# Kernel tuning notes

Measured on AMD Instinct MI355X. Metric: run time of the kernel, lower is better.

## Reference

```python
import jax, jax.numpy as jnp
import numpy as np

BS, C, H, W = 4, 128, 64, 64  # input_dim=128
INNER = 64


def setup_inputs() -> dict:
    key = jax.random.key(0)
    ks = jax.random.split(key, 9)
    s_in = 1.0 / np.sqrt(C)
    s_inner = 1.0 / np.sqrt(INNER)
    return {
        "inpt": jax.random.normal(ks[0], (BS, C, H, W), dtype=jnp.float32),
        "Wq": jax.random.normal(ks[1], (INNER, C), dtype=jnp.float32) * s_in,
        "bq": jax.random.normal(ks[2], (INNER,), dtype=jnp.float32) * 0.01,
        "Wk": jax.random.normal(ks[3], (INNER, C), dtype=jnp.float32) * s_in,
        "bk": jax.random.normal(ks[4], (INNER,), dtype=jnp.float32) * 0.01,
        "Wv": jax.random.normal(ks[5], (INNER, C), dtype=jnp.float32) * s_in,
        "bv": jax.random.normal(ks[6], (INNER,), dtype=jnp.float32) * 0.01,
        "Wo": jax.random.normal(ks[7], (C, INNER), dtype=jnp.float32) * s_inner,
        "bo": jax.random.normal(ks[8], (C,), dtype=jnp.float32) * 0.01,
    }


def reference(inpt, Wq, bq, Wk, bk, Wv, bv, Wo, bo):
    bs, c, h, w = inpt.shape
    L = h * w
    # [bs, C, H, W] -> [bs, L, C] (tokens = spatial positions)
    x = inpt.reshape(bs, c, L).transpose(0, 2, 1)
    q = jnp.einsum('blc,dc->bld', x, Wq) + bq  # [bs, L, INNER]
    k = jnp.einsum('blc,dc->bld', x, Wk) + bk
    v = jnp.einsum('blc,dc->bld', x, Wv) + bv
    # torch code divides by np.round(sqrt(d), 2); for d=64 this is exactly 8.0
    scale = jnp.float32(np.round(np.sqrt(q.shape[-1]), 2))
    scores = jnp.einsum('bld,bmd->blm', q, k) / scale  # [bs, L, L] score matrix
    factors = jax.nn.softmax(scores, axis=-1)
    ctx = jnp.einsum('blm,bmd->bld', factors, v)  # [bs, L, INNER]
    out = jnp.einsum('bld,cd->blc', ctx, Wo) + bo  # [bs, L, C]
    out = out.transpose(0, 2, 1).reshape(bs, c, h, w)
    return inpt + out
```

## Files before the change

### kernel.cpp

```cpp
#include <hip/hip_runtime.h>
#include <hip/hip_bf16.h>

typedef __bf16 bf16x8 __attribute__((ext_vector_type(8)));
typedef __bf16 bf16x4 __attribute__((ext_vector_type(4)));
typedef short  s16x4  __attribute__((ext_vector_type(4)));
typedef float  f32x4  __attribute__((ext_vector_type(4)));

#define MFMA32(a, b, c) __builtin_amdgcn_mfma_f32_16x16x32_bf16((a), (b), (c), 0, 0, 0)
#define MFMA16K(a, b, c) __builtin_amdgcn_mfma_f32_16x16x16bf16_1k((a), (b), (c), 0, 0, 0)

#if __has_builtin(__builtin_amdgcn_exp2f)
#define EXP2F(x) __builtin_amdgcn_exp2f(x)
#else
#define EXP2F(x) __expf(0.6931471805599453f * (x))
#endif

#define GL16(G, L)                                                            \
    __builtin_amdgcn_global_load_lds(                                         \
        (const __attribute__((address_space(1))) void*)(G),                   \
        (__attribute__((address_space(3))) void*)(L), 16, 0, 0)

#define SPLIT 4
#define QSCALE 0.18033688011112042f
#define BBOUND 12.0f


__global__ __launch_bounds__(256) void qkv_kernel(
    const float* __restrict__ inpt,
    const float* __restrict__ Wq, const float* __restrict__ bq,
    const float* __restrict__ Wk, const float* __restrict__ bk,
    const float* __restrict__ Wv, const float* __restrict__ bv,
    __bf16* __restrict__ Qws, __bf16* __restrict__ Kws, __bf16* __restrict__ VTws)
{
    __shared__ __align__(16) __bf16 xT[16 * 140];
    __shared__ __align__(16) __bf16 os[16 * 144];
    const int bid = blockIdx.x;
    const int b   = bid >> 8;
    const int l0  = (bid & 255) << 4;
    const int t   = threadIdx.x;

    {
        const int c = t >> 1, half = t & 1;
        const float* xin = inpt + ((size_t)(b * 128 + c)) * 4096 + l0 + half * 8;
        float4 v0 = *(const float4*)xin;
        float4 v1 = *(const float4*)(xin + 4);
        const int tok0 = half * 8;
        xT[(tok0 + 0) * 140 + c] = (__bf16)v0.x;
        xT[(tok0 + 1) * 140 + c] = (__bf16)v0.y;
        xT[(tok0 + 2) * 140 + c] = (__bf16)v0.z;
        xT[(tok0 + 3) * 140 + c] = (__bf16)v0.w;
        xT[(tok0 + 4) * 140 + c] = (__bf16)v1.x;
        xT[(tok0 + 5) * 140 + c] = (__bf16)v1.y;
        xT[(tok0 + 6) * 140 + c] = (__bf16)v1.z;
        xT[(tok0 + 7) * 140 + c] = (__bf16)v1.w;
    }
    __syncthreads();

    const int w    = t >> 6;
    const int lane = t & 63;
    const int quad = lane >> 4;
    const int l15  = lane & 15;

    f32x4 acc[3];
    #pragma unroll
    for (int j = 0; j < 3; ++j)
        #pragma unroll
        for (int r = 0; r < 4; ++r) acc[j][r] = 0.f;

    #pragma unroll
    for (int ks = 0; ks < 4; ++ks) {
        bf16x8 af = *(const bf16x8*)&xT[l15 * 140 + ks * 32 + quad * 8];
        #pragma unroll
        for (int j = 0; j < 3; ++j) {
            const int wn   = w * 3 + j;
            const int msel = wn >> 2;
            const float* W = (msel == 0) ? Wq : ((msel == 1) ? Wk : Wv);
            const float* Wp = W + ((wn & 3) * 16 + l15) * 128 + ks * 32 + quad * 8;
            float4 wa = *(const float4*)Wp;
            float4 wb = *(const float4*)(Wp + 4);
            bf16x8 bf;
            bf[0] = (__bf16)wa.x; bf[1] = (__bf16)wa.y;
            bf[2] = (__bf16)wa.z; bf[3] = (__bf16)wa.w;
            bf[4] = (__bf16)wb.x; bf[5] = (__bf16)wb.y;
            bf[6] = (__bf16)wb.z; bf[7] = (__bf16)wb.w;
            acc[j] = MFMA32(af, bf, acc[j]);
        }
    }

    #pragma unroll
    for (int j = 0; j < 3; ++j) {
        const int wn   = w * 3 + j;
        const int msel = wn >> 2;
        const int o0   = (wn & 3) * 16;
        const float* bb = (msel == 0) ? bq : ((msel == 1) ? bk : bv);
        float bias = bb[o0 + l15];
        if (msel < 2) {
            const float scl = (msel == 0) ? QSCALE : 1.0f;
            const int oc = wn * 16 + l15;
            #pragma unroll
            for (int r = 0; r < 4; ++r)
                os[(quad * 4 + r) * 144 + oc] = (__bf16)((acc[j][r] + bias) * scl);
        } else {
            const int d  = o0 + l15;
            const int kt = l0 >> 6;
            const int kc = (l0 >> 4) & 3;
            bf16x4 v;
            #pragma unroll
            for (int r = 0; r < 4; ++r) v[r] = (__bf16)(acc[j][r] + bias);
            *(bf16x4*)(VTws + (size_t)b * 262144 + kt * 4096
                       + d * 64 + quad * 16 + kc * 4) = v;
        }
    }
    __syncthreads();

    {
        const int tok = t >> 4, c = t & 15;
        bf16x8 v = *(const bf16x8*)&os[tok * 144 + c * 8];
        if (c < 8) {
            *(bf16x8*)(Qws + ((size_t)(b * 4096 + l0 + tok)) * 64 + c * 8) = v;
        } else {
            const int d8 = c - 8;
            __bf16* dst = Kws + (size_t)b * 262144
                + (l0 >> 6) * 4096
                + ((l0 >> 4) & 3) * 1024
                + (d8 >> 2) * 512
                + (d8 & 3) * 128
                + tok * 8;
            *(bf16x8*)dst = v;
        }
    }
}

__global__ __launch_bounds__(256, 4) void attn_kernel(
    const __bf16* __restrict__ Qws, const __bf16* __restrict__ Kws,
    const __bf16* __restrict__ VTws,
    __bf16* __restrict__ Ops, float* __restrict__ Lws)
{
    __shared__ __align__(16) __bf16 sbuf[2][4096];

    const int bid   = blockIdx.x;
    const int split = bid >> 8;
    const int qt    = bid & 255;
    const int b  = qt >> 6;
    const int l0 = (qt & 63) << 6;
    const int t    = threadIdx.x;
    const int w    = t >> 6;
    const int lane = t & 63;
    const int quad = lane >> 4;
    const int l15  = lane & 15;

    const __bf16* qptr = Qws + ((size_t)(b * 4096 + l0 + w * 16 + l15)) * 64 + quad * 8;
    bf16x8 qf0 = *(const bf16x8*)qptr;
    bf16x8 qf1 = *(const bf16x8*)(qptr + 32);

    f32x4 cfr[4];
    #pragma unroll
    for (int mt = 0; mt < 4; ++mt)
        #pragma unroll
        for (int r = 0; r < 4; ++r) cfr[mt][r] = 0.f;
    float l_run = 0.f;

    int voff[8];
    #pragma unroll
    for (int mt = 0; mt < 4; ++mt) {
        const int d = mt * 16 + l15;
        #pragma unroll
        for (int kc8 = 0; kc8 < 2; ++kc8)
            voff[kc8 * 4 + mt] = d * 64 + (((2 * quad + kc8) ^ (d & 7)) * 8);
    }

    const uint4* Vg = (const uint4*)(VTws + ((size_t)b << 18));
    const int rw = t >> 3, cw = (t & 7) ^ ((t >> 3) & 7);
    const uint4* vp = Vg + rw * 8 + cw + split * 8192;

    const __bf16* Kgl = Kws + ((size_t)b << 18)
                      + (size_t)(split * 16) * 4096 + lane * 8;

    union B4 { bf16x4 h; s16x4 s; };
    union V8 { bf16x8 v; s16x4 q[2]; };

    auto stageV = [&](__bf16* Bb) {
        GL16(vp,       Bb +        w * 512);
        GL16(vp + 256, Bb + 2048 + w * 512);
        vp += 512;
    };

    bf16x8 kfA[4][2], kfB[4][2];
    auto loadK = [&](bf16x8 (*kf)[2], int kt) {
        const __bf16* p = Kgl + (size_t)kt * 4096;
        #pragma unroll
        for (int nt = 0; nt < 4; ++nt) {
            kf[nt][0] = *(const bf16x8*)(p + nt * 1024);
            kf[nt][1] = *(const bf16x8*)(p + nt * 1024 + 512);
        }
    };

    auto tile_step = [&](const __bf16* __restrict__ B, bf16x8 (*kf)[2]) {
        B4 pk[4];
        float ps[4];
        #pragma unroll
        for (int nt = 0; nt < 4; ++nt) {
            f32x4 a = {-BBOUND, -BBOUND, -BBOUND, -BBOUND};
            a = MFMA32(kf[nt][0], qf0, a);
            a = MFMA32(kf[nt][1], qf1, a);
            float p0 = EXP2F(a[0]), p1 = EXP2F(a[1]);
            float p2 = EXP2F(a[2]), p3 = EXP2F(a[3]);
            pk[nt].h[0] = (__bf16)p0; pk[nt].h[1] = (__bf16)p1;
            pk[nt].h[2] = (__bf16)p2; pk[nt].h[3] = (__bf16)p3;
            ps[nt] = (p0 + p1) + (p2 + p3);
        }
        float psum = (ps[0] + ps[1]) + (ps[2] + ps[3]);
        psum += __shfl_xor(psum, 16);
        psum += __shfl_xor(psum, 32);
        l_run += psum;

        #pragma unroll
        for (int kc8 = 0; kc8 < 2; ++kc8) {
            #pragma unroll
            for (int mt = 0; mt < 4; ++mt) {
                V8 vv;
                vv.v = *(const bf16x8*)&B[voff[kc8 * 4 + mt]];
                cfr[mt] = MFMA16K(vv.q[0], pk[2 * kc8 + 0].s, cfr[mt]);
                cfr[mt] = MFMA16K(vv.q[1], pk[2 * kc8 + 1].s, cfr[mt]);
            }
        }
    };

    stageV(sbuf[0]);
    loadK(kfA, 0);

    for (int kt2 = 0; kt2 < 8; ++kt2) {
        __syncthreads();
        stageV(sbuf[1]);
        loadK(kfB, 2 * kt2 + 1);
        tile_step(sbuf[0], kfA);
        __syncthreads();
        if (kt2 < 7) {
            stageV(sbuf[0]);
            loadK(kfA, 2 * kt2 + 2);
        }
        tile_step(sbuf[1], kfB);
    }
    __syncthreads();

    {
        __bf16* tb = (__bf16*)sbuf + w * 1088;
        #pragma unroll
        for (int mt = 0; mt < 4; ++mt) {
            bf16x4 v;
            #pragma unroll
            for (int r = 0; r < 4; ++r) v[r] = (__bf16)cfr[mt][r];
            *(bf16x4*)&tb[l15 * 68 + mt * 16 + quad * 4] = v;
        }
        const int rowbase = (split * 4 + b) * 4096 + l0 + w * 16;
        #pragma unroll
        for (int h = 0; h < 2; ++h) {
            const int chunk = lane + h * 64;
            const int tok = chunk >> 3, c8 = chunk & 7;
            bf16x8 v = *(const bf16x8*)&tb[tok * 68 + c8 * 8];
            *(bf16x8*)(Ops + (size_t)(rowbase + tok) * 64 + c8 * 8) = v;
        }
        if (quad == 0) Lws[rowbase + l15] = l_run;
    }
}

__global__ __launch_bounds__(256) void outproj_kernel(
    const float* __restrict__ inpt,
    const __bf16* __restrict__ Ops, const float* __restrict__ Lws,
    const float* __restrict__ Wo, const float* __restrict__ bo,
    float* __restrict__ out)
{
    __shared__ __align__(16) __bf16 cx[16 * 72];
    const int bid = blockIdx.x;
    const int b   = bid >> 8;
    const int l0  = (bid & 255) << 4;
    const int t   = threadIdx.x;

    {
        const int token = t >> 4, d4 = (t & 15) << 2;
        const int rowb  = b * 4096 + l0 + token;
        float denom = 0.f;
        #pragma unroll
        for (int s = 0; s < SPLIT; ++s) denom += Lws[s * 16384 + rowb];
        const float inv = 1.f / denom;
        float ax = 0.f, ay = 0.f, az = 0.f, aw = 0.f;
        #pragma unroll
        for (int s = 0; s < SPLIT; ++s) {
            const bf16x4 v = *(const bf16x4*)(Ops
                + ((size_t)(s * 16384 + rowb)) * 64 + d4);
            ax += (float)v[0]; ay += (float)v[1];
            az += (float)v[2]; aw += (float)v[3];
        }
        bf16x4 pv;
        pv[0] = (__bf16)(ax * inv); pv[1] = (__bf16)(ay * inv);
        pv[2] = (__bf16)(az * inv); pv[3] = (__bf16)(aw * inv);
        *(bf16x4*)&cx[token * 72 + d4] = pv;
    }
    __syncthreads();

    const int w    = t >> 6;
    const int lane = t & 63;
    const int quad = lane >> 4;
    const int l15  = lane & 15;

    f32x4 acc[2];
    #pragma unroll
    for (int mi = 0; mi < 2; ++mi)
        #pragma unroll
        for (int r = 0; r < 4; ++r) acc[mi][r] = 0.f;

    #pragma unroll
    for (int ks = 0; ks < 2; ++ks) {
        bf16x8 bfrag = *(const bf16x8*)&cx[l15 * 72 + ks * 32 + quad * 8];
        #pragma unroll
        for (int mi = 0; mi < 2; ++mi) {
            const int crow = (w * 2 + mi) * 16 + l15;
            const float* Wp = Wo + crow * 64 + ks * 32 + quad * 8;
            float4 wa = *(const float4*)Wp;
            float4 wb = *(const float4*)(Wp + 4);
            bf16x8 afrag;
            afrag[0] = (__bf16)wa.x; afrag[1] = (__bf16)wa.y;
            afrag[2] = (__bf16)wa.z; afrag[3] = (__bf16)wa.w;
            afrag[4] = (__bf16)wb.x; afrag[5] = (__bf16)wb.y;
            afrag[6] = (__bf16)wb.z; afrag[7] = (__bf16)wb.w;
            acc[mi] = MFMA32(afrag, bfrag, acc[mi]);
        }
    }

    #pragma unroll
    for (int mi = 0; mi < 2; ++mi) {
        #pragma unroll
        for (int r = 0; r < 4; ++r) {
            const int c = (w * 2 + mi) * 16 + quad * 4 + r;
            const size_t addr = ((size_t)(b * 128 + c)) * 4096 + l0 + l15;
            out[addr] = inpt[addr] + bo[c] + acc[mi][r];
        }
    }
}

extern "C" void kernel_launch(void* const* d_in, const int* in_sizes, int n_in,
                              void* d_out, int out_size, void* d_ws, size_t ws_size,
                              hipStream_t stream)
{
    const float* inpt = (const float*)d_in[0];
    const float* Wq   = (const float*)d_in[1];
    const float* bq   = (const float*)d_in[2];
    const float* Wk   = (const float*)d_in[3];
    const float* bk   = (const float*)d_in[4];
    const float* Wv   = (const float*)d_in[5];
    const float* bv   = (const float*)d_in[6];
    const float* Wo   = (const float*)d_in[7];
    const float* bo   = (const float*)d_in[8];
    float* out = (float*)d_out;

    char* ws = (char*)d_ws;
    const size_t MB = (size_t)1 << 20;
    __bf16* Qws  = (__bf16*)(ws + 0 * MB);
    __bf16* Kws  = (__bf16*)(ws + 2 * MB);
    __bf16* VTws = (__bf16*)(ws + 4 * MB);
    __bf16* Ops  = (__bf16*)(ws + 6 * MB);
    float*  Lws  = (float*)(ws + 16 * MB);

    qkv_kernel<<<1024, 256, 0, stream>>>(inpt, Wq, bq, Wk, bk, Wv, bv, Qws, Kws, VTws);
    attn_kernel<<<SPLIT * 256, 256, 0, stream>>>(Qws, Kws, VTws, Ops, Lws);
    outproj_kernel<<<1024, 256, 0, stream>>>(inpt, Ops, Lws, Wo, bo, out);
}
```

Before: 124.6 us.

## Store V in MFMA fragment order and read K/V directly from global

The qkv kernel now writes V in a layout that matches the MFMA operand fragments. The attention kernel can then load V per lane straight from global memory, so the LDS double-buffering, its barriers and the async global-to-LDS copies are gone. The split-K factor goes from 4 to 8 with a higher occupancy bound, and the partial outputs are stored in fragment order without an LDS transpose. Outproj reads them back with the matching indices. The cost is more split partials to reduce and no explicit prefetch, so the kernel relies on occupancy to hide global latency.

Result: slower. 275.4 us (+120.9%).

```diff
diff --git a/kernel.cpp b/kernel.cpp
--- a/kernel.cpp
+++ b/kernel.cpp
@@ -15,12 +15,7 @@
 #define EXP2F(x) __expf(0.6931471805599453f * (x))
 #endif
 
-#define GL16(G, L)                                                            \
-    __builtin_amdgcn_global_load_lds(                                         \
-        (const __attribute__((address_space(1))) void*)(G),                   \
-        (__attribute__((address_space(3))) void*)(L), 16, 0, 0)
-
-#define SPLIT 4
+#define SPLIT 8
 #define QSCALE 0.18033688011112042f
 #define BBOUND 12.0f
 
@@ -101,14 +96,14 @@
             for (int r = 0; r < 4; ++r)
                 os[(quad * 4 + r) * 144 + oc] = (__bf16)((acc[j][r] + bias) * scl);
         } else {
-            const int d  = o0 + l15;
-            const int kt = l0 >> 6;
-            const int kc = (l0 >> 4) & 3;
+            const int mt  = wn & 3;
+            const int kc8 = (l0 >> 5) & 1;
+            const int i2b = ((l0 >> 4) & 1) * 4;
             bf16x4 v;
             #pragma unroll
             for (int r = 0; r < 4; ++r) v[r] = (__bf16)(acc[j][r] + bias);
-            *(bf16x4*)(VTws + (size_t)b * 262144 + kt * 4096
-                       + d * 64 + quad * 16 + kc * 4) = v;
+            *(bf16x4*)(VTws + (size_t)b * 262144 + (l0 >> 6) * 4096
+                       + mt * 1024 + kc8 * 512 + (quad * 16 + l15) * 8 + i2b) = v;
         }
     }
     __syncthreads();
@@ -131,13 +126,11 @@
     }
 }
 
-__global__ __launch_bounds__(256, 4) void attn_kernel(
+__global__ __launch_bounds__(256, 8) void attn_kernel(
     const __bf16* __restrict__ Qws, const __bf16* __restrict__ Kws,
     const __bf16* __restrict__ VTws,
     __bf16* __restrict__ Ops, float* __restrict__ Lws)
 {
-    __shared__ __align__(16) __bf16 sbuf[2][4096];
-
     const int bid   = blockIdx.x;
     const int split = bid >> 8;
     const int qt    = bid & 255;
@@ -160,49 +153,25 @@
         for (int r = 0; r < 4; ++r) cfr[mt][r] = 0.f;
     float l_run = 0.f;
 
-    int voff[8];
-    #pragma unroll
-    for (int mt = 0; mt < 4; ++mt) {
-        const int d = mt * 16 + l15;
-        #pragma unroll
-        for (int kc8 = 0; kc8 < 2; ++kc8)
-            voff[kc8 * 4 + mt] = d * 64 + (((2 * quad + kc8) ^ (d & 7)) * 8);
-    }
-
-    const uint4* Vg = (const uint4*)(VTws + ((size_t)b << 18));
-    const int rw = t >> 3, cw = (t & 7) ^ ((t >> 3) & 7);
-    const uint4* vp = Vg + rw * 8 + cw + split * 8192;
-
-    const __bf16* Kgl = Kws + ((size_t)b << 18)
-                      + (size_t)(split * 16) * 4096 + lane * 8;
+    const __bf16* Kt = Kws  + ((size_t)b << 18) + (size_t)split * 8 * 4096 + lane * 8;
+    const __bf16* Vt = VTws + ((size_t)b << 18) + (size_t)split * 8 * 4096 + lane * 8;
 
     union B4 { bf16x4 h; s16x4 s; };
     union V8 { bf16x8 v; s16x4 q[2]; };
 
-    auto stageV = [&](__bf16* Bb) {
-        GL16(vp,       Bb +        w * 512);
-        GL16(vp + 256, Bb + 2048 + w * 512);
-        vp += 512;
-    };
-
-    bf16x8 kfA[4][2], kfB[4][2];
-    auto loadK = [&](bf16x8 (*kf)[2], int kt) {
-        const __bf16* p = Kgl + (size_t)kt * 4096;
-        #pragma unroll
-        for (int nt = 0; nt < 4; ++nt) {
-            kf[nt][0] = *(const bf16x8*)(p + nt * 1024);
-            kf[nt][1] = *(const bf16x8*)(p + nt * 1024 + 512);
-        }
-    };
-
-    auto tile_step = [&](const __bf16* __restrict__ B, bf16x8 (*kf)[2]) {
+    for (int kt = 0; kt < 8; ++kt) {
+        const __bf16* Kp = Kt + kt * 4096;
+        const __bf16* Vp = Vt + kt * 4096;
+
         B4 pk[4];
         float ps[4];
         #pragma unroll
         for (int nt = 0; nt < 4; ++nt) {
+            bf16x8 kf0 = *(const bf16x8*)(Kp + nt * 1024);
+            bf16x8 kf1 = *(const bf16x8*)(Kp + nt * 1024 + 512);
             f32x4 a = {-BBOUND, -BBOUND, -BBOUND, -BBOUND};
-            a = MFMA32(kf[nt][0], qf0, a);
-            a = MFMA32(kf[nt][1], qf1, a);
+            a = MFMA32(kf0, qf0, a);
+            a = MFMA32(kf1, qf1, a);
             float p0 = EXP2F(a[0]), p1 = EXP2F(a[1]);
             float p2 = EXP2F(a[2]), p3 = EXP2F(a[3]);
             pk[nt].h[0] = (__bf16)p0; pk[nt].h[1] = (__bf16)p1;
@@ -219,48 +188,24 @@
             #pragma unroll
             for (int mt = 0; mt < 4; ++mt) {
                 V8 vv;
-                vv.v = *(const bf16x8*)&B[voff[kc8 * 4 + mt]];
+                vv.v = *(const bf16x8*)(Vp + mt * 1024 + kc8 * 512);
                 cfr[mt] = MFMA16K(vv.q[0], pk[2 * kc8 + 0].s, cfr[mt]);
                 cfr[mt] = MFMA16K(vv.q[1], pk[2 * kc8 + 1].s, cfr[mt]);
             }
         }
-    };
-
-    stageV(sbuf[0]);
-    loadK(kfA, 0);
-
-    for (int kt2 = 0; kt2 < 8; ++kt2) {
-        __syncthreads();
-        stageV(sbuf[1]);
-        loadK(kfB, 2 * kt2 + 1);
-        tile_step(sbuf[0], kfA);
-        __syncthreads();
-        if (kt2 < 7) {
-            stageV(sbuf[0]);
-            loadK(kfA, 2 * kt2 + 2);
-        }
-        tile_step(sbuf[1], kfB);
-    }
-    __syncthreads();
+    }
 
     {
-        __bf16* tb = (__bf16*)sbuf + w * 1088;
+        const int qb = (l0 >> 4) + w;
+        __bf16* ob = Ops + (((size_t)((split * 4 + b) * 256 + qb)) << 10) + lane * 4;
         #pragma unroll
         for (int mt = 0; mt < 4; ++mt) {
             bf16x4 v;
             #pragma unroll
             for (int r = 0; r < 4; ++r) v[r] = (__bf16)cfr[mt][r];
-            *(bf16x4*)&tb[l15 * 68 + mt * 16 + quad * 4] = v;
-        }
-        const int rowbase = (split * 4 + b) * 4096 + l0 + w * 16;
-        #pragma unroll
-        for (int h = 0; h < 2; ++h) {
-            const int chunk = lane + h * 64;
-            const int tok = chunk >> 3, c8 = chunk & 7;
-            bf16x8 v = *(const bf16x8*)&tb[tok * 68 + c8 * 8];
-            *(bf16x8*)(Ops + (size_t)(rowbase + tok) * 64 + c8 * 8) = v;
-        }
-        if (quad == 0) Lws[rowbase + l15] = l_run;
+            *(bf16x4*)(ob + mt * 256) = v;
+        }
+        if (quad == 0) Lws[(split * 4 + b) * 4096 + l0 + w * 16 + l15] = l_run;
     }
 }
 
@@ -273,7 +218,8 @@
     __shared__ __align__(16) __bf16 cx[16 * 72];
     const int bid = blockIdx.x;
     const int b   = bid >> 8;
-    const int l0  = (bid & 255) << 4;
+    const int qb  = bid & 255;
+    const int l0  = qb << 4;
     const int t   = threadIdx.x;
 
     {
@@ -283,11 +229,13 @@
         #pragma unroll
         for (int s = 0; s < SPLIT; ++s) denom += Lws[s * 16384 + rowb];
         const float inv = 1.f / denom;
+        const int mt     = d4 >> 4;
+        const int lane_f = ((d4 >> 2) & 3) * 16 + token;
         float ax = 0.f, ay = 0.f, az = 0.f, aw = 0.f;
         #pragma unroll
         for (int s = 0; s < SPLIT; ++s) {
             const bf16x4 v = *(const bf16x4*)(Ops
-                + ((size_t)(s * 16384 + rowb)) * 64 + d4);
+                + (((size_t)((s * 4 + b) * 256 + qb)) << 10) + mt * 256 + lane_f * 4);
             ax += (float)v[0]; ay += (float)v[1];
             az += (float)v[2]; aw += (float)v[3];
         }
@@ -359,7 +307,7 @@
     __bf16* Kws  = (__bf16*)(ws + 2 * MB);
     __bf16* VTws = (__bf16*)(ws + 4 * MB);
     __bf16* Ops  = (__bf16*)(ws + 6 * MB);
-    float*  Lws  = (float*)(ws + 16 * MB);
+    float*  Lws  = (float*)(ws + 24 * MB);
 
     qkv_kernel<<<1024, 256, 0, stream>>>(inpt, Wq, bq, Wk, bk, Wv, bv, Qws, Kws, VTws);
     attn_kernel<<<SPLIT * 256, 256, 0, stream>>>(Qws, Kws, VTws, Ops, Lws);
```
